# Performance work log

Hardware: AMD Instinct MI355X
Metric: run time of the kernel (lower is better)

## Reference

```python
import jax, jax.numpy as jnp
import numpy as np

B, S, H2 = 32, 8192, 256  # batch, max_enc_steps, 2*hidden_dim
INIT_STD = 1e-4           # trunc_norm_init_std


def setup_inputs() -> dict:
    key = jax.random.key(0)
    k1, k2, k3 = jax.random.split(key, 3)
    h_d_t = jax.random.normal(k1, (B, H2), dtype=jnp.float32)
    h_enc = jax.random.normal(k2, (B, S, H2), dtype=jnp.float32)
    enc_padding_mask = jnp.ones((B, S), dtype=jnp.float32)
    sum_exp_att = jnp.ones((B, S), dtype=jnp.float32)
    # Bilinear weight (attn_dim=1 squeezed): (2H, 2H), trunc-normal init
    W = jax.random.normal(k3, (H2, H2), dtype=jnp.float32) * INIT_STD
    return {"h_d_t": h_d_t, "h_enc": h_enc, "enc_padding_mask": enc_padding_mask,
            "sum_exp_att": sum_exp_att, "W": W}


def reference(h_d_t, h_enc, enc_padding_mask, sum_exp_att, W):
    # Batched bilinear scores: score[b,s] = h_d_t[b] @ W @ h_enc[b,s]
    # replaces the per-timestep nn.Bilinear loop with one fused contraction.
    scores = jnp.einsum('bd,de,bse->bs', h_d_t, W, h_enc)  # (B, S)
    exp_att = jnp.exp(scores)
    # intra-temporal normalization by accumulated past exp attention
    att = exp_att / sum_exp_att
    new_sum_exp_att = sum_exp_att + exp_att
    # mask pads and renormalize
    alphat_e = att * enc_padding_mask
    alphat_e = alphat_e / jnp.sum(alphat_e, axis=1, keepdims=True)
    # context vector: weighted sum over encoder states
    ct_e = jnp.einsum('bs,bsd->bd', alphat_e, h_enc)  # (B, 2H)
    return ct_e, alphat_e, new_sum_exp_att
```

## Files before the change

kernel.cpp:

```cpp
#include <hip/hip_runtime.h>

#define B_ 32
#define S_ 8192
#define H_ 256

#define SPB 128

__global__ __launch_bounds__(256) void gemv_hdtW(
    const float* __restrict__ hdt,
    const float* __restrict__ W,
    float* __restrict__ v)
{
    const int b  = blockIdx.x;
    const int ec = blockIdx.y;
    const int d  = threadIdx.x;

    __shared__ float lh[32];
    if (d < 32) lh[d] = hdt[b * H_ + ec * 32 + d];
    __syncthreads();

    float acc = 0.f;
    const float* Wp = W + (size_t)(ec * 32) * H_ + d;
#pragma unroll
    for (int e = 0; e < 32; ++e) acc = fmaf(lh[e], Wp[(size_t)e * H_], acc);

    atomicAdd(&v[b * H_ + d], acc);
}

__global__ __launch_bounds__(256, 5) void attn_main(
    const float* __restrict__ v,
    const float* __restrict__ h_enc,
    const float* __restrict__ sum_exp,
    const float* __restrict__ mask,
    float* __restrict__ out_alphat,
    float* __restrict__ out_newsum,
    float* __restrict__ denom,
    float* __restrict__ ct_un)
{
    const int b    = blockIdx.y;
    const int tid  = threadIdx.x;
    const int lane = tid & 63;
    const int wave = tid >> 6;
    const int sub  = lane & 15;
    const int grp  = lane >> 4;
    const int pid  = wave * 4 + grp;
    const int s0   = blockIdx.x * SPB;

    __shared__ float lmult[SPB];
    __shared__ float lse[SPB];
    __shared__ float lalpha[SPB];
    __shared__ float lnew[SPB];
    __shared__ __align__(16) float lct[16][H_];
    __shared__ float lden[16];

    if (tid < SPB) {
        const float se = sum_exp[(size_t)b * S_ + s0 + tid];
        const float mk = mask[(size_t)b * S_ + s0 + tid];
        lse[tid]   = se;
        lmult[tid] = mk / se;
    }
    __syncthreads();

    const float4* v4 = reinterpret_cast<const float4*>(v + b * H_);
    const float4 vf0 = v4[0 * 16 + sub];
    const float4 vf1 = v4[1 * 16 + sub];
    const float4 vf2 = v4[2 * 16 + sub];
    const float4 vf3 = v4[3 * 16 + sub];

    const float* __restrict__ hb = h_enc + (size_t)b * S_ * H_;

    float4 ct0 = {0.f,0.f,0.f,0.f}, ct1 = {0.f,0.f,0.f,0.f};
    float4 ct2 = {0.f,0.f,0.f,0.f}, ct3 = {0.f,0.f,0.f,0.f};
    float  den = 0.f;

#pragma unroll 2
    for (int i = 0; i < SPB / 16; ++i) {
        const int lr = i * 16 + wave * 4 + grp;
        const float4* h4 = reinterpret_cast<const float4*>(hb + (size_t)(s0 + lr) * H_);
        const float4 h0 = h4[0 * 16 + sub];
        const float4 h1 = h4[1 * 16 + sub];
        const float4 h2 = h4[2 * 16 + sub];
        const float4 h3 = h4[3 * 16 + sub];

        float dot;
        dot = fmaf(vf0.x, h0.x, fmaf(vf0.y, h0.y, fmaf(vf0.z, h0.z, vf0.w * h0.w)));
        dot = fmaf(vf1.x, h1.x, fmaf(vf1.y, h1.y, fmaf(vf1.z, h1.z, fmaf(vf1.w, h1.w, dot))));
        dot = fmaf(vf2.x, h2.x, fmaf(vf2.y, h2.y, fmaf(vf2.z, h2.z, fmaf(vf2.w, h2.w, dot))));
        dot = fmaf(vf3.x, h3.x, fmaf(vf3.y, h3.y, fmaf(vf3.z, h3.z, fmaf(vf3.w, h3.w, dot))));

        dot += __shfl_xor(dot, 1, 16);
        dot += __shfl_xor(dot, 2, 16);
        dot += __shfl_xor(dot, 4, 16);
        dot += __shfl_xor(dot, 8, 16);

        const float e   = __expf(dot);
        const float att = e * lmult[lr];
        if (sub == 0) {
            lalpha[lr] = att;
            lnew[lr]   = lse[lr] + e;
        }
        den += att;
        ct0.x = fmaf(att, h0.x, ct0.x); ct0.y = fmaf(att, h0.y, ct0.y);
        ct0.z = fmaf(att, h0.z, ct0.z); ct0.w = fmaf(att, h0.w, ct0.w);
        ct1.x = fmaf(att, h1.x, ct1.x); ct1.y = fmaf(att, h1.y, ct1.y);
        ct1.z = fmaf(att, h1.z, ct1.z); ct1.w = fmaf(att, h1.w, ct1.w);
        ct2.x = fmaf(att, h2.x, ct2.x); ct2.y = fmaf(att, h2.y, ct2.y);
        ct2.z = fmaf(att, h2.z, ct2.z); ct2.w = fmaf(att, h2.w, ct2.w);
        ct3.x = fmaf(att, h3.x, ct3.x); ct3.y = fmaf(att, h3.y, ct3.y);
        ct3.z = fmaf(att, h3.z, ct3.z); ct3.w = fmaf(att, h3.w, ct3.w);
    }

    float4* dst = reinterpret_cast<float4*>(&lct[pid][0]);
    dst[0 * 16 + sub] = ct0;
    dst[1 * 16 + sub] = ct1;
    dst[2 * 16 + sub] = ct2;
    dst[3 * 16 + sub] = ct3;
    if (sub == 0) lden[pid] = den;
    __syncthreads();

    float tot = 0.f;
#pragma unroll
    for (int p = 0; p < 16; ++p) tot += lct[p][tid];
    atomicAdd(&ct_un[b * H_ + tid], tot);

    if (tid == 0) {
        float d = 0.f;
#pragma unroll
        for (int p = 0; p < 16; ++p) d += lden[p];
        atomicAdd(&denom[b], d);
    }

    if (tid < SPB) {
        out_alphat[(size_t)b * S_ + s0 + tid] = lalpha[tid];
        out_newsum[(size_t)b * S_ + s0 + tid] = lnew[tid];
    }
}

__global__ __launch_bounds__(256) void finalize(
    const float* __restrict__ denom,
    const float* __restrict__ ct_un,
    float* __restrict__ out_ct,
    float* __restrict__ out_alphat)
{
    const int idx = blockIdx.x * blockDim.x + threadIdx.x;
    if (idx < B_ * H_) {
        out_ct[idx] = ct_un[idx] / denom[idx >> 8];
    } else {
        const int p = idx - B_ * H_;
        if (p < B_ * S_) {
            out_alphat[p] = out_alphat[p] / denom[p >> 13];
        }
    }
}

extern "C" void kernel_launch(void* const* d_in, const int* in_sizes, int n_in,
                              void* d_out, int out_size, void* d_ws, size_t ws_size,
                              hipStream_t stream) {
    const float* h_d_t   = (const float*)d_in[0];
    const float* h_enc   = (const float*)d_in[1];
    const float* mask    = (const float*)d_in[2];
    const float* sum_exp = (const float*)d_in[3];
    const float* W       = (const float*)d_in[4];

    float* out        = (float*)d_out;
    float* out_ct     = out;
    float* out_alphat = out + B_ * H_;
    float* out_newsum = out + B_ * H_ + B_ * S_;

    float* ws    = (float*)d_ws;
    float* denom = ws;
    float* ct_un = ws + B_;
    float* v     = ws + B_ + B_ * H_;
    hipMemsetAsync(d_ws, 0, (size_t)(B_ + 2 * B_ * H_) * sizeof(float), stream);

    gemv_hdtW<<<dim3(B_, 8), 256, 0, stream>>>(h_d_t, W, v);
    attn_main<<<dim3(S_ / SPB, B_), 256, 0, stream>>>(v, h_enc, sum_exp, mask,
                                                      out_alphat, out_newsum, denom, ct_un);
    const int fin_n = B_ * H_ + B_ * S_;
    finalize<<<(fin_n + 255) / 256, 256, 0, stream>>>(denom, ct_un, out_ct, out_alphat);
}
```

Measured before the change: 374.8 us.

## Replace atomics and memset with partial-sum buffers, DPP reductions, two rows per iteration

```diff
diff --git a/kernel.cpp b/kernel.cpp
--- a/kernel.cpp
+++ b/kernel.cpp
@@ -5,11 +5,21 @@
 #define H_ 256
 
 #define SPB 128
+#define NBLK (S_ / SPB)
+
+__device__ __forceinline__ float row16_allsum(float x) {
+    float t;
+    t = __int_as_float(__builtin_amdgcn_update_dpp(0, __float_as_int(x), 0x121, 0xF, 0xF, false)); x += t;
+    t = __int_as_float(__builtin_amdgcn_update_dpp(0, __float_as_int(x), 0x122, 0xF, 0xF, false)); x += t;
+    t = __int_as_float(__builtin_amdgcn_update_dpp(0, __float_as_int(x), 0x124, 0xF, 0xF, false)); x += t;
+    t = __int_as_float(__builtin_amdgcn_update_dpp(0, __float_as_int(x), 0x128, 0xF, 0xF, false)); x += t;
+    return x;
+}
 
 __global__ __launch_bounds__(256) void gemv_hdtW(
     const float* __restrict__ hdt,
     const float* __restrict__ W,
-    float* __restrict__ v)
+    float* __restrict__ v_part)
 {
     const int b  = blockIdx.x;
     const int ec = blockIdx.y;
@@ -24,27 +34,28 @@
 #pragma unroll
     for (int e = 0; e < 32; ++e) acc = fmaf(lh[e], Wp[(size_t)e * H_], acc);
 
-    atomicAdd(&v[b * H_ + d], acc);
-}
-
-__global__ __launch_bounds__(256, 5) void attn_main(
-    const float* __restrict__ v,
+    v_part[(size_t)(ec * B_ + b) * H_ + d] = acc;
+}
+
+__global__ __launch_bounds__(256) void attn_main(
+    const float* __restrict__ v_part,
     const float* __restrict__ h_enc,
     const float* __restrict__ sum_exp,
     const float* __restrict__ mask,
     float* __restrict__ out_alphat,
     float* __restrict__ out_newsum,
-    float* __restrict__ denom,
-    float* __restrict__ ct_un)
+    float* __restrict__ part_den,
+    float* __restrict__ part_ct)
 {
     const int b    = blockIdx.y;
+    const int bx   = blockIdx.x;
     const int tid  = threadIdx.x;
     const int lane = tid & 63;
     const int wave = tid >> 6;
     const int sub  = lane & 15;
     const int grp  = lane >> 4;
     const int pid  = wave * 4 + grp;
-    const int s0   = blockIdx.x * SPB;
+    const int s0   = bx * SPB;
 
     __shared__ float lmult[SPB];
     __shared__ float lse[SPB];
@@ -61,73 +72,92 @@
     }
     __syncthreads();
 
-    const float4* v4 = reinterpret_cast<const float4*>(v + b * H_);
-    const float4 vf0 = v4[0 * 16 + sub];
-    const float4 vf1 = v4[1 * 16 + sub];
-    const float4 vf2 = v4[2 * 16 + sub];
-    const float4 vf3 = v4[3 * 16 + sub];
+    const float4* vp4 = reinterpret_cast<const float4*>(v_part);
+    float4 vf0 = {0,0,0,0}, vf1 = {0,0,0,0}, vf2 = {0,0,0,0}, vf3 = {0,0,0,0};
+#pragma unroll
+    for (int ec = 0; ec < 8; ++ec) {
+        const int base = (ec * B_ + b) * (H_ / 4);
+        float4 p;
+        p = vp4[base + 0*16 + sub]; vf0.x += p.x; vf0.y += p.y; vf0.z += p.z; vf0.w += p.w;
+        p = vp4[base + 1*16 + sub]; vf1.x += p.x; vf1.y += p.y; vf1.z += p.z; vf1.w += p.w;
+        p = vp4[base + 2*16 + sub]; vf2.x += p.x; vf2.y += p.y; vf2.z += p.z; vf2.w += p.w;
+        p = vp4[base + 3*16 + sub]; vf3.x += p.x; vf3.y += p.y; vf3.z += p.z; vf3.w += p.w;
+    }
 
     const float* __restrict__ hb = h_enc + (size_t)b * S_ * H_;
 
-    float4 ct0 = {0.f,0.f,0.f,0.f}, ct1 = {0.f,0.f,0.f,0.f};
-    float4 ct2 = {0.f,0.f,0.f,0.f}, ct3 = {0.f,0.f,0.f,0.f};
+    float4 ct0 = {0,0,0,0}, ct1 = {0,0,0,0}, ct2 = {0,0,0,0}, ct3 = {0,0,0,0};
     float  den = 0.f;
 
 #pragma unroll 2
-    for (int i = 0; i < SPB / 16; ++i) {
-        const int lr = i * 16 + wave * 4 + grp;
-        const float4* h4 = reinterpret_cast<const float4*>(hb + (size_t)(s0 + lr) * H_);
-        const float4 h0 = h4[0 * 16 + sub];
-        const float4 h1 = h4[1 * 16 + sub];
-        const float4 h2 = h4[2 * 16 + sub];
-        const float4 h3 = h4[3 * 16 + sub];
-
-        float dot;
-        dot = fmaf(vf0.x, h0.x, fmaf(vf0.y, h0.y, fmaf(vf0.z, h0.z, vf0.w * h0.w)));
-        dot = fmaf(vf1.x, h1.x, fmaf(vf1.y, h1.y, fmaf(vf1.z, h1.z, fmaf(vf1.w, h1.w, dot))));
-        dot = fmaf(vf2.x, h2.x, fmaf(vf2.y, h2.y, fmaf(vf2.z, h2.z, fmaf(vf2.w, h2.w, dot))));
-        dot = fmaf(vf3.x, h3.x, fmaf(vf3.y, h3.y, fmaf(vf3.z, h3.z, fmaf(vf3.w, h3.w, dot))));
-
-        dot += __shfl_xor(dot, 1, 16);
-        dot += __shfl_xor(dot, 2, 16);
-        dot += __shfl_xor(dot, 4, 16);
-        dot += __shfl_xor(dot, 8, 16);
-
-        const float e   = __expf(dot);
-        const float att = e * lmult[lr];
+    for (int i = 0; i < SPB / 32; ++i) {
+        const int ra = i * 32 + pid * 2;
+        const int rb = ra + 1;
+        const float4* h4a = reinterpret_cast<const float4*>(hb + (size_t)(s0 + ra) * H_);
+        const float4* h4b = reinterpret_cast<const float4*>(hb + (size_t)(s0 + rb) * H_);
+        const float4 a0 = h4a[0*16 + sub], a1 = h4a[1*16 + sub];
+        const float4 a2 = h4a[2*16 + sub], a3 = h4a[3*16 + sub];
+        const float4 b0 = h4b[0*16 + sub], b1 = h4b[1*16 + sub];
+        const float4 b2 = h4b[2*16 + sub], b3 = h4b[3*16 + sub];
+
+        float da, db;
+        da = fmaf(vf0.x, a0.x, fmaf(vf0.y, a0.y, fmaf(vf0.z, a0.z, vf0.w * a0.w)));
+        da = fmaf(vf1.x, a1.x, fmaf(vf1.y, a1.y, fmaf(vf1.z, a1.z, fmaf(vf1.w, a1.w, da))));
+        da = fmaf(vf2.x, a2.x, fmaf(vf2.y, a2.y, fmaf(vf2.z, a2.z, fmaf(vf2.w, a2.w, da))));
+        da = fmaf(vf3.x, a3.x, fmaf(vf3.y, a3.y, fmaf(vf3.z, a3.z, fmaf(vf3.w, a3.w, da))));
+        db = fmaf(vf0.x, b0.x, fmaf(vf0.y, b0.y, fmaf(vf0.z, b0.z, vf0.w * b0.w)));
+        db = fmaf(vf1.x, b1.x, fmaf(vf1.y, b1.y, fmaf(vf1.z, b1.z, fmaf(vf1.w, b1.w, db))));
+        db = fmaf(vf2.x, b2.x, fmaf(vf2.y, b2.y, fmaf(vf2.z, b2.z, fmaf(vf2.w, b2.w, db))));
+        db = fmaf(vf3.x, b3.x, fmaf(vf3.y, b3.y, fmaf(vf3.z, b3.z, fmaf(vf3.w, b3.w, db))));
+
+        da = row16_allsum(da);
+        db = row16_allsum(db);
+
+        const float ea = __expf(da);
+        const float eb = __expf(db);
+        const float atta = ea * lmult[ra];
+        const float attb = eb * lmult[rb];
         if (sub == 0) {
-            lalpha[lr] = att;
-            lnew[lr]   = lse[lr] + e;
+            lalpha[ra] = atta;  lnew[ra] = lse[ra] + ea;
+            lalpha[rb] = attb;  lnew[rb] = lse[rb] + eb;
         }
-        den += att;
-        ct0.x = fmaf(att, h0.x, ct0.x); ct0.y = fmaf(att, h0.y, ct0.y);
-        ct0.z = fmaf(att, h0.z, ct0.z); ct0.w = fmaf(att, h0.w, ct0.w);
-        ct1.x = fmaf(att, h1.x, ct1.x); ct1.y = fmaf(att, h1.y, ct1.y);
-        ct1.z = fmaf(att, h1.z, ct1.z); ct1.w = fmaf(att, h1.w, ct1.w);
-        ct2.x = fmaf(att, h2.x, ct2.x); ct2.y = fmaf(att, h2.y, ct2.y);
-        ct2.z = fmaf(att, h2.z, ct2.z); ct2.w = fmaf(att, h2.w, ct2.w);
-        ct3.x = fmaf(att, h3.x, ct3.x); ct3.y = fmaf(att, h3.y, ct3.y);
-        ct3.z = fmaf(att, h3.z, ct3.z); ct3.w = fmaf(att, h3.w, ct3.w);
+        den += atta + attb;
+        ct0.x = fmaf(atta, a0.x, fmaf(attb, b0.x, ct0.x));
+        ct0.y = fmaf(atta, a0.y, fmaf(attb, b0.y, ct0.y));
+        ct0.z = fmaf(atta, a0.z, fmaf(attb, b0.z, ct0.z));
+        ct0.w = fmaf(atta, a0.w, fmaf(attb, b0.w, ct0.w));
+        ct1.x = fmaf(atta, a1.x, fmaf(attb, b1.x, ct1.x));
+        ct1.y = fmaf(atta, a1.y, fmaf(attb, b1.y, ct1.y));
+        ct1.z = fmaf(atta, a1.z, fmaf(attb, b1.z, ct1.z));
+        ct1.w = fmaf(atta, a1.w, fmaf(attb, b1.w, ct1.w));
+        ct2.x = fmaf(atta, a2.x, fmaf(attb, b2.x, ct2.x));
+        ct2.y = fmaf(atta, a2.y, fmaf(attb, b2.y, ct2.y));
+        ct2.z = fmaf(atta, a2.z, fmaf(attb, b2.z, ct2.z));
+        ct2.w = fmaf(atta, a2.w, fmaf(attb, b2.w, ct2.w));
+        ct3.x = fmaf(atta, a3.x, fmaf(attb, b3.x, ct3.x));
+        ct3.y = fmaf(atta, a3.y, fmaf(attb, b3.y, ct3.y));
+        ct3.z = fmaf(atta, a3.z, fmaf(attb, b3.z, ct3.z));
+        ct3.w = fmaf(atta, a3.w, fmaf(attb, b3.w, ct3.w));
     }
 
     float4* dst = reinterpret_cast<float4*>(&lct[pid][0]);
-    dst[0 * 16 + sub] = ct0;
-    dst[1 * 16 + sub] = ct1;
-    dst[2 * 16 + sub] = ct2;
-    dst[3 * 16 + sub] = ct3;
+    dst[0*16 + sub] = ct0;
+    dst[1*16 + sub] = ct1;
+    dst[2*16 + sub] = ct2;
+    dst[3*16 + sub] = ct3;
     if (sub == 0) lden[pid] = den;
     __syncthreads();
 
     float tot = 0.f;
 #pragma unroll
     for (int p = 0; p < 16; ++p) tot += lct[p][tid];
-    atomicAdd(&ct_un[b * H_ + tid], tot);
+    part_ct[((size_t)b * NBLK + bx) * H_ + tid] = tot;
 
     if (tid == 0) {
         float d = 0.f;
 #pragma unroll
         for (int p = 0; p < 16; ++p) d += lden[p];
-        atomicAdd(&denom[b], d);
+        part_den[b * NBLK + bx] = d;
     }
 
     if (tid < SPB) {
@@ -137,20 +167,32 @@
 }
 
 __global__ __launch_bounds__(256) void finalize(
-    const float* __restrict__ denom,
-    const float* __restrict__ ct_un,
+    const float* __restrict__ part_den,
+    const float* __restrict__ part_ct,
     float* __restrict__ out_ct,
     float* __restrict__ out_alphat)
 {
-    const int idx = blockIdx.x * blockDim.x + threadIdx.x;
-    if (idx < B_ * H_) {
-        out_ct[idx] = ct_un[idx] / denom[idx >> 8];
-    } else {
-        const int p = idx - B_ * H_;
-        if (p < B_ * S_) {
-            out_alphat[p] = out_alphat[p] / denom[p >> 13];
-        }
-    }
+    const int b   = blockIdx.x;
+    const int tid = threadIdx.x;
+
+    __shared__ float pd[NBLK];
+    if (tid < NBLK) pd[tid] = part_den[b * NBLK + tid];
+    __syncthreads();
+
+    float den = 0.f;
+#pragma unroll
+    for (int k = 0; k < NBLK; ++k) den += pd[k];
+    const float inv = 1.f / den;
+
+    float ct = 0.f;
+    const float* pc = part_ct + (size_t)b * NBLK * H_ + tid;
+#pragma unroll 8
+    for (int k = 0; k < NBLK; ++k) ct += pc[(size_t)k * H_];
+    out_ct[b * H_ + tid] = ct * inv;
+
+    float* oa = out_alphat + (size_t)b * S_;
+#pragma unroll 4
+    for (int s = tid; s < S_; s += 256) oa[s] *= inv;
 }
 
 extern "C" void kernel_launch(void* const* d_in, const int* in_sizes, int n_in,
@@ -167,15 +209,14 @@
     float* out_alphat = out + B_ * H_;
     float* out_newsum = out + B_ * H_ + B_ * S_;
 
-    float* ws    = (float*)d_ws;
-    float* denom = ws;
-    float* ct_un = ws + B_;
-    float* v     = ws + B_ + B_ * H_;
-    hipMemsetAsync(d_ws, 0, (size_t)(B_ + 2 * B_ * H_) * sizeof(float), stream);
-
-    gemv_hdtW<<<dim3(B_, 8), 256, 0, stream>>>(h_d_t, W, v);
-    attn_main<<<dim3(S_ / SPB, B_), 256, 0, stream>>>(v, h_enc, sum_exp, mask,
-                                                      out_alphat, out_newsum, denom, ct_un);
-    const int fin_n = B_ * H_ + B_ * S_;
-    finalize<<<(fin_n + 255) / 256, 256, 0, stream>>>(denom, ct_un, out_ct, out_alphat);
-}
+    float* ws       = (float*)d_ws;
+    float* v_part   = ws;
+    float* part_den = v_part + 8 * B_ * H_;
+    float* part_ct  = part_den + B_ * NBLK;
+
+    gemv_hdtW<<<dim3(B_, 8), 256, 0, stream>>>(h_d_t, W, v_part);
+    attn_main<<<dim3(NBLK, B_), 256, 0, stream>>>(v_part, h_enc, sum_exp, mask,
+                                                  out_alphat, out_newsum,
+                                                  part_den, part_ct);
+    finalize<<<B_, 256, 0, stream>>>(part_den, part_ct, out_ct, out_alphat);
+}
```

Result: no change. 376.4 us (+0.4%).
